# Optimization experiments

Hardware: AMD Instinct MI355X
Metric: run time of the kernel (lower is better)

## Reference

```python
import jax, jax.numpy as jnp
import numpy as np
from jax import lax

DIM = 256
NUM_HEADS = 8
HEAD_DIM = DIM // NUM_HEADS
SCALE = HEAD_DIM ** -0.5
DBZ_THRESHOLD = 15.0
DILATION = 1


def setup_inputs() -> dict:
    key = jax.random.key(0)
    k_x, k_dbz, k_qkv, k_pw, k_pb = jax.random.split(key, 5)
    B, T, H, W, C = 1, 4, 32, 32, DIM
    x = jax.random.normal(k_x, (B, T, H, W, C), dtype=jnp.float32)
    dbz_values = jax.random.uniform(k_dbz, (B, T, H, W, 1), dtype=jnp.float32) * 75.0
    s = 1.0 / np.sqrt(C)
    qkv_w = jax.random.uniform(k_qkv, (3 * C, C), minval=-s, maxval=s, dtype=jnp.float32)
    proj_w = jax.random.uniform(k_pw, (C, C), minval=-s, maxval=s, dtype=jnp.float32)
    proj_b = jax.random.uniform(k_pb, (C,), minval=-s, maxval=s, dtype=jnp.float32)
    return {"x": x, "dbz_values": dbz_values, "qkv_w": qkv_w, "proj_w": proj_w, "proj_b": proj_b}


def _keep_mask(dbz_values):
    # valid precipitation tokens
    valid = dbz_values[..., 0] >= DBZ_THRESHOLD  # (B,T,H,W) bool
    B, T, H, W = valid.shape
    ksz = 2 * DILATION + 1
    vf = valid.astype(jnp.float32).reshape(B * T, H, W)
    # morphological dilation == max-pool (stride 1, zero-pad). Padding with -inf is
    # equivalent here since every window contains >=1 real pixel (value >= 0).
    dilated = lax.reduce_window(vf, -jnp.inf, lax.max,
                                (1, ksz, ksz), (1, 1, 1),
                                [(0, 0), (DILATION, DILATION), (DILATION, DILATION)])
    boundary = ((dilated > 0.5) != (vf > 0.5)).reshape(B, T, H, W)
    return valid | boundary  # hybrid keep mask


def reference(x, dbz_values, qkv_w, proj_w, proj_b):
    B, T, H, W, C = x.shape
    keep = _keep_mask(dbz_values).reshape(-1)          # (N,) over all B*T*H*W tokens
    x_flat = x.reshape(-1, C)                          # (N,C)
    N = x_flat.shape[0]

    # QKV projection (no bias)
    qkv = (x_flat @ qkv_w.T).reshape(N, 3, NUM_HEADS, HEAD_DIM)
    q = jnp.transpose(qkv[:, 0], (1, 0, 2))           # (h,N,d)
    k = jnp.transpose(qkv[:, 1], (1, 0, 2))
    v = jnp.transpose(qkv[:, 2], (1, 0, 2))

    # dense attention among kept tokens == masked attention over all tokens:
    # mask non-kept KEYS with -inf; zero out non-kept QUERY outputs afterwards.
    attn = jnp.einsum('hnd,hmd->hnm', q, k) * SCALE    # (h,N,N)
    attn = jnp.where(keep[None, None, :], attn, -jnp.inf)
    attn = jax.nn.softmax(attn, axis=-1)
    out = jnp.einsum('hnm,hmd->hnd', attn, v)          # (h,N,d)
    out = jnp.transpose(out, (1, 0, 2)).reshape(N, C)
    out = out @ proj_w.T + proj_b
    out = jnp.where(keep[:, None], out, 0.0).reshape(B, T, H, W, C)
    return out + x  # residual
```

## Files before the change

kernel.cpp:

```cpp
#include <hip/hip_runtime.h>
#include <hip/hip_bf16.h>

#define N_TOK 4096
#define NH 8
#define HD 32
#define CDIM 256
#define QKV_N 768
#define VT_STRIDE 4128
#define XB_STRIDE 272
#define SCALE_F 0.17677669529663687f
#define LOG2E   1.4426950408889634f

typedef float  f32x4  __attribute__((ext_vector_type(4)));
typedef int    i32x4  __attribute__((ext_vector_type(4)));
typedef short  s16x4  __attribute__((ext_vector_type(4)));
typedef __bf16 bf16x8 __attribute__((ext_vector_type(8)));

union FragI { i32x4 i; bf16x8 b; };
union FragH { struct { s16x4 lo, hi; } s; bf16x8 b; };

__device__ inline int pack_bf16_trunc(float a, float b) {
  return (int)__builtin_amdgcn_perm(__builtin_bit_cast(unsigned, b),
                                    __builtin_bit_cast(unsigned, a),
                                    0x07060302u);
}

#define SEG_X 1048576
#define SEG_W (SEG_X + 196608)
#define SEG_P (SEG_W + 65536)
#define SEG_M (SEG_P + 4096)
__global__ __launch_bounds__(256) void fused_prep(const float* __restrict__ x,
                                                  const float* __restrict__ qkv_w,
                                                  const float* __restrict__ proj_w,
                                                  const float* __restrict__ dbz,
                                                  __bf16* __restrict__ xb,
                                                  __bf16* __restrict__ wqkvb,
                                                  __bf16* __restrict__ wprojb,
                                                  float* __restrict__ bias,
                                                  int* __restrict__ keepi) {
  int gid = blockIdx.x * 256 + threadIdx.x;
  if (gid < SEG_X) {
    xb[(gid >> 8) * XB_STRIDE + (gid & 255)] = (__bf16)x[gid];
  } else if (gid < SEG_W) {
    int i = gid - SEG_X;
    float s = ((i >> 8) < 256) ? (SCALE_F * LOG2E) : 1.0f;
    wqkvb[(i >> 8) * XB_STRIDE + (i & 255)] = (__bf16)(qkv_w[i] * s);
  } else if (gid < SEG_P) {
    int i = gid - SEG_W;
    wprojb[(i >> 8) * XB_STRIDE + (i & 255)] = (__bf16)proj_w[i];
  } else if (gid < SEG_M) {
    int n = gid - SEG_P;
    int t = n >> 10, rc = n & 1023, r = rc >> 5, c = rc & 31;
    bool keep = false;
    #pragma unroll
    for (int dr = -1; dr <= 1; dr++)
      #pragma unroll
      for (int dc = -1; dc <= 1; dc++) {
        int rr = r + dr, cc = c + dc;
        if (rr >= 0 && rr < 32 && cc >= 0 && cc < 32)
          keep = keep || (dbz[t * 1024 + rr * 32 + cc] >= 15.0f);
      }
    bias[n]  = keep ? 0.0f : -30000.0f;
    keepi[n] = keep ? 1 : 0;
  }
}

__global__ __launch_bounds__(256) void qkv_gemm(const __bf16* __restrict__ xb,
                                                const __bf16* __restrict__ wb,
                                                __bf16* __restrict__ qb,
                                                __bf16* __restrict__ kb,
                                                __bf16* __restrict__ vt) {
  int wave = threadIdx.x >> 6, lane = threadIdx.x & 63;
  int quad = lane >> 4, l16 = lane & 15;
  int m0 = blockIdx.x * 64 + wave * 16;
  int n0 = blockIdx.y * 64;

  const __bf16* xrow = xb + (size_t)(m0 + l16) * XB_STRIDE + quad * 8;
  const __bf16* wrow = wb + (size_t)(n0 + l16) * XB_STRIDE + quad * 8;

  FragI xc, wc[4];
  xc.i = *(const i32x4*)(xrow);
  #pragma unroll
  for (int nt = 0; nt < 4; nt++)
    wc[nt].i = *(const i32x4*)(wrow + (size_t)nt * 16 * XB_STRIDE);

  f32x4 acc[4] = {};
  for (int kk = 0; kk < CDIM; kk += 32) {
    int kn = (kk + 32 < CDIM) ? kk + 32 : 0;
    FragI xn, wn[4];
    xn.i = *(const i32x4*)(xrow + kn);
    #pragma unroll
    for (int nt = 0; nt < 4; nt++)
      wn[nt].i = *(const i32x4*)(wrow + (size_t)nt * 16 * XB_STRIDE + kn);
    #pragma unroll
    for (int nt = 0; nt < 4; nt++)
      acc[nt] = __builtin_amdgcn_mfma_f32_16x16x32_bf16(wc[nt].b, xc.b, acc[nt], 0, 0, 0);
    xc = xn;
    #pragma unroll
    for (int nt = 0; nt < 4; nt++) wc[nt] = wn[nt];
  }
  int m = m0 + l16;
  #pragma unroll
  for (int nt = 0; nt < 4; nt++) {
    int cbase = n0 + nt * 16 + quad * 4;
    int which = cbase >> 8, rem = cbase & 255, hd = rem >> 5, d0 = rem & 31;
    if (which < 2) {
      union { s16x4 s; __bf16 h[4]; } u;
      #pragma unroll
      for (int r = 0; r < 4; r++) u.h[r] = (__bf16)acc[nt][r];
      __bf16* dst = (which == 0 ? qb : kb) + ((size_t)hd * N_TOK + m) * HD + d0;
      *(s16x4*)dst = u.s;
    } else {
      #pragma unroll
      for (int r = 0; r < 4; r++)
        vt[(size_t)(hd * HD + d0 + r) * VT_STRIDE + m] = (__bf16)acc[nt][r];
    }
  }
}

__global__ __launch_bounds__(256, 2) void attn_kernel(const __bf16* __restrict__ qb,
                                                      const __bf16* __restrict__ kb,
                                                      const __bf16* __restrict__ vt,
                                                      const float* __restrict__ bias,
                                                      __bf16* __restrict__ ob) {
  __shared__ float red_o[4][64][34];
  __shared__ float red_l[4][64];

  int b = blockIdx.x;
  int head = b & 7, qx = b >> 3;
  int wave = threadIdx.x >> 6, lane = threadIdx.x & 63;
  int quad = lane >> 4, l16 = lane & 15;
  int q0 = qx * 64;

  const __bf16* qh = qb + (size_t)head * N_TOK * HD;
  const __bf16* kh = kb + (size_t)head * N_TOK * HD;
  const __bf16* vh = vt + (size_t)head * HD * VT_STRIDE;

  FragI qf[4];
  #pragma unroll
  for (int g = 0; g < 4; g++)
    qf[g].i = *(const i32x4*)(qh + (size_t)(q0 + g * 16 + l16) * HD + quad * 8);

  FragI ones;
  #pragma unroll
  for (int j = 0; j < 8; j++) ones.b[j] = (__bf16)1.0f;

  f32x4 o_lo[4] = {}, o_hi[4] = {}, lacc[4] = {};

  FragI ka_c, kb_c;
  f32x4 ba_c, bb_c;
  FragH vlo_c, vhi_c;
  {
    int k0 = wave * 32;
    ka_c.i = *(const i32x4*)(kh + (size_t)(k0 + l16) * HD + quad * 8);
    kb_c.i = *(const i32x4*)(kh + (size_t)(k0 + 16 + l16) * HD + quad * 8);
    ba_c = *(const f32x4*)(bias + k0 + quad * 4);
    bb_c = *(const f32x4*)(bias + k0 + 16 + quad * 4);
    const __bf16* vp = vh + (size_t)l16 * VT_STRIDE + k0 + quad * 4;
    vlo_c.s.lo = *(const s16x4*)(vp);
    vlo_c.s.hi = *(const s16x4*)(vp + 16);
    const __bf16* vp2 = vh + (size_t)(16 + l16) * VT_STRIDE + k0 + quad * 4;
    vhi_c.s.lo = *(const s16x4*)(vp2);
    vhi_c.s.hi = *(const s16x4*)(vp2 + 16);
  }

  for (int t = 0; t < 32; t++) {
    int kc = wave * 32 + t * 128;
    int kn = (t < 31) ? kc + 128 : wave * 32;

    FragI ka_n, kb_n;
    f32x4 ba_n, bb_n;
    FragH vlo_n, vhi_n;
    ka_n.i = *(const i32x4*)(kh + (size_t)(kn + l16) * HD + quad * 8);
    kb_n.i = *(const i32x4*)(kh + (size_t)(kn + 16 + l16) * HD + quad * 8);
    ba_n = *(const f32x4*)(bias + kn + quad * 4);
    bb_n = *(const f32x4*)(bias + kn + 16 + quad * 4);
    {
      const __bf16* vp = vh + (size_t)l16 * VT_STRIDE + kn + quad * 4;
      vlo_n.s.lo = *(const s16x4*)(vp);
      vlo_n.s.hi = *(const s16x4*)(vp + 16);
      const __bf16* vp2 = vh + (size_t)(16 + l16) * VT_STRIDE + kn + quad * 4;
      vhi_n.s.lo = *(const s16x4*)(vp2);
      vhi_n.s.hi = *(const s16x4*)(vp2 + 16);
    }

    f32x4 sa[4], sb[4];
    #pragma unroll
    for (int g = 0; g < 4; g++) {
      sa[g] = __builtin_amdgcn_mfma_f32_16x16x32_bf16(ka_c.b, qf[g].b, ba_c, 0, 0, 0);
      sb[g] = __builtin_amdgcn_mfma_f32_16x16x32_bf16(kb_c.b, qf[g].b, bb_c, 0, 0, 0);
    }

    FragI pf[4];
    #pragma unroll
    for (int g = 0; g < 4; g++) {
      float e0 = __builtin_amdgcn_exp2f(sa[g][0]);
      float e1 = __builtin_amdgcn_exp2f(sa[g][1]);
      float e2 = __builtin_amdgcn_exp2f(sa[g][2]);
      float e3 = __builtin_amdgcn_exp2f(sa[g][3]);
      float e4 = __builtin_amdgcn_exp2f(sb[g][0]);
      float e5 = __builtin_amdgcn_exp2f(sb[g][1]);
      float e6 = __builtin_amdgcn_exp2f(sb[g][2]);
      float e7 = __builtin_amdgcn_exp2f(sb[g][3]);
      pf[g].i[0] = pack_bf16_trunc(e0, e1);
      pf[g].i[1] = pack_bf16_trunc(e2, e3);
      pf[g].i[2] = pack_bf16_trunc(e4, e5);
      pf[g].i[3] = pack_bf16_trunc(e6, e7);
    }

    #pragma unroll
    for (int g = 0; g < 4; g++) {
      o_lo[g] = __builtin_amdgcn_mfma_f32_16x16x32_bf16(vlo_c.b, pf[g].b, o_lo[g], 0, 0, 0);
      o_hi[g] = __builtin_amdgcn_mfma_f32_16x16x32_bf16(vhi_c.b, pf[g].b, o_hi[g], 0, 0, 0);
      lacc[g] = __builtin_amdgcn_mfma_f32_16x16x32_bf16(ones.b, pf[g].b, lacc[g], 0, 0, 0);
    }

    ka_c = ka_n; kb_c = kb_n; ba_c = ba_n; bb_c = bb_n;
    vlo_c = vlo_n; vhi_c = vhi_n;
  }

  #pragma unroll
  for (int g = 0; g < 4; g++) {
    int q = g * 16 + l16;
    #pragma unroll
    for (int r = 0; r < 4; r++) {
      red_o[wave][q][quad * 4 + r]      = o_lo[g][r];
      red_o[wave][q][16 + quad * 4 + r] = o_hi[g][r];
    }
    if (quad == 0) red_l[wave][q] = lacc[g][0];
  }
  __syncthreads();

  int q = wave * 16 + l16;
  float lt = red_l[0][q] + red_l[1][q] + red_l[2][q] + red_l[3][q];
  float inv = 1.0f / lt;
  f32x4 slo = {0.f, 0.f, 0.f, 0.f}, shi = {0.f, 0.f, 0.f, 0.f};
  #pragma unroll
  for (int src = 0; src < 4; src++) {
    #pragma unroll
    for (int r = 0; r < 4; r++) {
      slo[r] += red_o[src][q][quad * 4 + r];
      shi[r] += red_o[src][q][16 + quad * 4 + r];
    }
  }
  union { s16x4 s; __bf16 h[4]; } u1, u2;
  #pragma unroll
  for (int r = 0; r < 4; r++) {
    u1.h[r] = (__bf16)(slo[r] * inv);
    u2.h[r] = (__bf16)(shi[r] * inv);
  }
  __bf16* orow = ob + (size_t)(q0 + q) * XB_STRIDE + head * HD;
  *(s16x4*)(orow + quad * 4)      = u1.s;
  *(s16x4*)(orow + 16 + quad * 4) = u2.s;
}

__global__ __launch_bounds__(256) void proj_gemm(const __bf16* __restrict__ ob,
                                                 const __bf16* __restrict__ wb,
                                                 const float* __restrict__ pb,
                                                 const int* __restrict__ keepi,
                                                 const float* __restrict__ x,
                                                 float* __restrict__ out) {
  int wave = threadIdx.x >> 6, lane = threadIdx.x & 63;
  int quad = lane >> 4, l16 = lane & 15;
  int m0 = blockIdx.x * 64 + wave * 16;
  int n0 = blockIdx.y * 64;

  const __bf16* arow = ob + (size_t)(m0 + l16) * XB_STRIDE + quad * 8;
  const __bf16* wrow = wb + (size_t)(n0 + l16) * XB_STRIDE + quad * 8;

  FragI ac, wc[4];
  ac.i = *(const i32x4*)(arow);
  #pragma unroll
  for (int nt = 0; nt < 4; nt++)
    wc[nt].i = *(const i32x4*)(wrow + (size_t)nt * 16 * XB_STRIDE);

  f32x4 acc[4] = {};
  for (int kk = 0; kk < CDIM; kk += 32) {
    int kn = (kk + 32 < CDIM) ? kk + 32 : 0;
    FragI an, wn[4];
    an.i = *(const i32x4*)(arow + kn);
    #pragma unroll
    for (int nt = 0; nt < 4; nt++)
      wn[nt].i = *(const i32x4*)(wrow + (size_t)nt * 16 * XB_STRIDE + kn);
    #pragma unroll
    for (int nt = 0; nt < 4; nt++)
      acc[nt] = __builtin_amdgcn_mfma_f32_16x16x32_bf16(wc[nt].b, ac.b, acc[nt], 0, 0, 0);
    ac = an;
    #pragma unroll
    for (int nt = 0; nt < 4; nt++) wc[nt] = wn[nt];
  }
  int m = m0 + l16;
  int keep = keepi[m];
  #pragma unroll
  for (int nt = 0; nt < 4; nt++) {
    int c0 = n0 + nt * 16 + quad * 4;
    #pragma unroll
    for (int r = 0; r < 4; r++) {
      float v = acc[nt][r] + pb[c0 + r];
      v = keep ? v : 0.0f;
      out[(size_t)m * CDIM + c0 + r] = v + x[(size_t)m * CDIM + c0 + r];
    }
  }
}

extern "C" void kernel_launch(void* const* d_in, const int* in_sizes, int n_in,
                              void* d_out, int out_size, void* d_ws, size_t ws_size,
                              hipStream_t stream) {
  const float* x      = (const float*)d_in[0];
  const float* dbz    = (const float*)d_in[1];
  const float* qkv_w  = (const float*)d_in[2];
  const float* proj_w = (const float*)d_in[3];
  const float* proj_b = (const float*)d_in[4];
  float* out = (float*)d_out;

  char* w = (char*)d_ws;
  __bf16* xb     = (__bf16*)(w);
  __bf16* qb     = (__bf16*)(w + (3u << 20));
  __bf16* kb     = (__bf16*)(w + (5u << 20));
  __bf16* vt     = (__bf16*)(w + (7u << 20));
  __bf16* ob     = (__bf16*)(w + (9u << 20) + (512u << 10));
  __bf16* wqkvb  = (__bf16*)(w + (12u << 20));
  __bf16* wprojb = (__bf16*)(w + (12u << 20) + (512u << 10));
  float*  bias   = (float*)(w + (13u << 20));
  int*    keepi  = (int*)(w + (13u << 20) + 16384);

  fused_prep<<<dim3(SEG_M / 256), dim3(256), 0, stream>>>(
      x, qkv_w, proj_w, dbz, xb, wqkvb, wprojb, bias, keepi);
  qkv_gemm<<<dim3(N_TOK / 64, QKV_N / 64), dim3(256), 0, stream>>>(
      xb, wqkvb, qb, kb, vt);
  attn_kernel<<<dim3((N_TOK / 64) * NH), dim3(256), 0, stream>>>(
      qb, kb, vt, bias, ob);
  proj_gemm<<<dim3(N_TOK / 64, CDIM / 64), dim3(256), 0, stream>>>(
      ob, wprojb, proj_b, keepi, x, out);
}
```

Before: 112.8 us.

## Split attention key loop across eight waves with two-stage LDS reduction

```diff
diff --git a/kernel.cpp b/kernel.cpp
--- a/kernel.cpp
+++ b/kernel.cpp
@@ -118,7 +118,7 @@
   }
 }
 
-__global__ __launch_bounds__(256, 2) void attn_kernel(const __bf16* __restrict__ qb,
+__global__ __launch_bounds__(512, 4) void attn_kernel(const __bf16* __restrict__ qb,
                                                       const __bf16* __restrict__ kb,
                                                       const __bf16* __restrict__ vt,
                                                       const float* __restrict__ bias,
@@ -164,9 +164,9 @@
     vhi_c.s.hi = *(const s16x4*)(vp2 + 16);
   }
 
-  for (int t = 0; t < 32; t++) {
-    int kc = wave * 32 + t * 128;
-    int kn = (t < 31) ? kc + 128 : wave * 32;
+  for (int t = 0; t < 16; t++) {
+    int kc = wave * 32 + t * 256;
+    int kn = (t < 15) ? kc + 256 : wave * 32;
 
     FragI ka_n, kb_n;
     f32x4 ba_n, bb_n;
@@ -219,39 +219,69 @@
     vlo_c = vlo_n; vhi_c = vhi_n;
   }
 
-  #pragma unroll
-  for (int g = 0; g < 4; g++) {
-    int q = g * 16 + l16;
+  if (wave >= 4) {
+    int w = wave - 4;
+    #pragma unroll
+    for (int g = 0; g < 4; g++) {
+      int q = g * 16 + l16;
+      #pragma unroll
+      for (int r = 0; r < 4; r++) {
+        red_o[w][q][quad * 4 + r]      = o_lo[g][r];
+        red_o[w][q][16 + quad * 4 + r] = o_hi[g][r];
+      }
+      if (quad == 0) red_l[w][q] = lacc[g][0];
+    }
+  }
+  __syncthreads();
+  if (wave < 4) {
+    #pragma unroll
+    for (int g = 0; g < 4; g++) {
+      int q = g * 16 + l16;
+      #pragma unroll
+      for (int r = 0; r < 4; r++) {
+        o_lo[g][r] += red_o[wave][q][quad * 4 + r];
+        o_hi[g][r] += red_o[wave][q][16 + quad * 4 + r];
+      }
+      if (quad == 0) lacc[g][0] += red_l[wave][q];
+    }
+  }
+  __syncthreads();
+  if (wave < 4) {
+    #pragma unroll
+    for (int g = 0; g < 4; g++) {
+      int q = g * 16 + l16;
+      #pragma unroll
+      for (int r = 0; r < 4; r++) {
+        red_o[wave][q][quad * 4 + r]      = o_lo[g][r];
+        red_o[wave][q][16 + quad * 4 + r] = o_hi[g][r];
+      }
+      if (quad == 0) red_l[wave][q] = lacc[g][0];
+    }
+  }
+  __syncthreads();
+  if (wave < 4) {
+    int q = wave * 16 + l16;
+    float lt = red_l[0][q] + red_l[1][q] + red_l[2][q] + red_l[3][q];
+    float inv = 1.0f / lt;
+    f32x4 slo = {0.f, 0.f, 0.f, 0.f}, shi = {0.f, 0.f, 0.f, 0.f};
+    #pragma unroll
+    for (int src = 0; src < 4; src++) {
+      #pragma unroll
+      for (int r = 0; r < 4; r++) {
+        slo[r] += red_o[src][q][quad * 4 + r];
+        shi[r] += red_o[src][q][16 + quad * 4 + r];
+      }
+    }
+    union { s16x4 s; __bf16 h[4]; } u1, u2;
     #pragma unroll
     for (int r = 0; r < 4; r++) {
-      red_o[wave][q][quad * 4 + r]      = o_lo[g][r];
-      red_o[wave][q][16 + quad * 4 + r] = o_hi[g][r];
-    }
-    if (quad == 0) red_l[wave][q] = lacc[g][0];
-  }
-  __syncthreads();
-
-  int q = wave * 16 + l16;
-  float lt = red_l[0][q] + red_l[1][q] + red_l[2][q] + red_l[3][q];
-  float inv = 1.0f / lt;
-  f32x4 slo = {0.f, 0.f, 0.f, 0.f}, shi = {0.f, 0.f, 0.f, 0.f};
-  #pragma unroll
-  for (int src = 0; src < 4; src++) {
-    #pragma unroll
-    for (int r = 0; r < 4; r++) {
-      slo[r] += red_o[src][q][quad * 4 + r];
-      shi[r] += red_o[src][q][16 + quad * 4 + r];
-    }
-  }
-  union { s16x4 s; __bf16 h[4]; } u1, u2;
-  #pragma unroll
-  for (int r = 0; r < 4; r++) {
-    u1.h[r] = (__bf16)(slo[r] * inv);
-    u2.h[r] = (__bf16)(shi[r] * inv);
-  }
-  __bf16* orow = ob + (size_t)(q0 + q) * XB_STRIDE + head * HD;
-  *(s16x4*)(orow + quad * 4)      = u1.s;
-  *(s16x4*)(orow + 16 + quad * 4) = u2.s;
+      u1.h[r] = (__bf16)(slo[r] * inv);
+      u2.h[r] = (__bf16)(shi[r] * inv);
+    }
+    __bf16* orow = ob + (size_t)(q0 + q) * XB_STRIDE + head * HD;
+    *(s16x4*)(orow + quad * 4)      = u1.s;
+    *(s16x4*)(orow + 16 + quad * 4) = u2.s;
+  }
 }
 
 __global__ __launch_bounds__(256) void proj_gemm(const __bf16* __restrict__ ob,
@@ -328,7 +358,7 @@
       x, qkv_w, proj_w, dbz, xb, wqkvb, wprojb, bias, keepi);
   qkv_gemm<<<dim3(N_TOK / 64, QKV_N / 64), dim3(256), 0, stream>>>(
       xb, wqkvb, qb, kb, vt);
-  attn_kernel<<<dim3((N_TOK / 64) * NH), dim3(256), 0, stream>>>(
+  attn_kernel<<<dim3((N_TOK / 64) * NH), dim3(512), 0, stream>>>(
       qb, kb, vt, bias, ob);
   proj_gemm<<<dim3(N_TOK / 64, CDIM / 64), dim3(256), 0, stream>>>(
       ob, wprojb, proj_b, keepi, x, out);
```

After: 113.8 us. No clear change (+0.9%).
